# Performance work log

Hardware: AMD Instinct MI355X
Metric: run time of the kernel (lower is better)

## Reference

```python
import jax, jax.numpy as jnp
import numpy as np

B, S, V, E, H = 1024, 64, 32, 256, 512
META = 13


def setup_inputs() -> dict:
    key = jax.random.key(0)
    ks = jax.random.split(key, 12)
    return {
        "image_representation": jax.random.normal(ks[0], (B, META), jnp.float32),
        "messages": jax.random.randint(ks[1], (B, S), 0, V),
        "embedding": jax.random.normal(ks[2], (V, E), jnp.float32) * 0.1,
        "w_ih": jax.random.normal(ks[3], (4 * H, E), jnp.float32) * 0.02,
        "w_hh": jax.random.normal(ks[4], (4 * H, H), jnp.float32) * 0.02,
        "b_ih": jnp.zeros((4 * H,), jnp.float32),
        "b_hh": jnp.zeros((4 * H,), jnp.float32).at[H:2 * H].set(1.0),
        "proc_w": jax.random.normal(ks[5], (H, META), jnp.float32) * 0.1,
        "proc_b": jnp.zeros((H,), jnp.float32),
        "w1": jax.random.normal(ks[6], (H, 2 * H), jnp.float32) * 0.02,
        "b1": jnp.zeros((H,), jnp.float32),
        "w2": jax.random.normal(ks[7], (2, H), jnp.float32) * 0.02,
        "b2": jnp.zeros((2,), jnp.float32),
    }


def _lstm_run(emb_tbe, w_ih, w_hh, b_ih, b_hh):
    # emb_tbe: [S, B, E]; PyTorch LSTMCell gate order: i, f, g, o
    Bn = emb_tbe.shape[1]
    Hn = w_hh.shape[1]

    def step(carry, x_t):
        h, c = carry
        gates = x_t @ w_ih.T + b_ih + h @ w_hh.T + b_hh  # [B, 4H]
        i, f, g, o = jnp.split(gates, 4, axis=-1)
        c = jax.nn.sigmoid(f) * c + jax.nn.sigmoid(i) * jnp.tanh(g)
        h = jax.nn.sigmoid(o) * jnp.tanh(c)
        return (h, c), None

    init = (jnp.zeros((Bn, Hn), emb_tbe.dtype), jnp.zeros((Bn, Hn), emb_tbe.dtype))
    (h, _), _ = jax.lax.scan(step, init, emb_tbe)
    return h


def reference(image_representation, messages, embedding, w_ih, w_hh, b_ih, b_hh,
              proc_w, proc_b, w1, b1, w2, b2):
    emb = embedding[messages]                       # [B, S, E]
    h = _lstm_run(jnp.transpose(emb, (1, 0, 2)), w_ih, w_hh, b_ih, b_hh)  # [B, H]
    img = image_representation @ proc_w.T + proc_b  # [B, H]
    combined = jnp.concatenate([h, img], axis=1)    # [B, 2H]
    hidden = jax.nn.relu(combined @ w1.T + b1)
    prediction = hidden @ w2.T + b2                 # [B, 2]
    return prediction, emb
```

## Files before the change

### kernel.cpp

```cpp
#include <hip/hip_runtime.h>

typedef __attribute__((ext_vector_type(8))) short bf16x8;
typedef __attribute__((ext_vector_type(4))) float f32x4;
typedef unsigned long long u64;

__device__ __forceinline__ unsigned short f2bf(float x) {
    union { float f; unsigned u; } c; c.f = x;
    unsigned u = c.u + 0x7fffu + ((c.u >> 16) & 1u);
    return (unsigned short)(u >> 16);
}
__device__ __forceinline__ unsigned pack2(float a, float b) {
    return (unsigned)f2bf(a) | ((unsigned)f2bf(b) << 16);
}
__device__ __forceinline__ float sigm(float x) { return 1.f / (1.f + __expf(-x)); }
__device__ __forceinline__ float tanh_(float x) { return 1.f - 2.f / (__expf(2.f * x) + 1.f); }

#define ALOAD(p)     __hip_atomic_load((p), __ATOMIC_RELAXED, __HIP_MEMORY_SCOPE_AGENT)
#define ASTORE(p, v) __hip_atomic_store((p), (v), __ATOMIC_RELAXED, __HIP_MEMORY_SCOPE_AGENT)

__global__ __launch_bounds__(256) void prep_k(
    const float* __restrict__ emb, const float* __restrict__ w_ih,
    const float* __restrict__ b_ih, const float* __restrict__ b_hh,
    const float* __restrict__ w_hh, const float* __restrict__ w1,
    const float* __restrict__ imgr, const float* __restrict__ procw,
    const float* __restrict__ procb,
    float* __restrict__ table, unsigned short* __restrict__ Wp,
    unsigned short* __restrict__ w1p, unsigned short* __restrict__ imgb)
{
    int wg = blockIdx.x, tid = threadIdx.x;
    if (wg < 256) {
        int id = wg * 256 + tid;
        int v = id >> 11, c = id & 2047;
        int c7 = c & 127, tt = c >> 7;
        int srow = ((c7 >> 4) & 3) * 512 + tt * 32 + ((c7 >> 6) & 1) * 16 + (c7 & 15);
        const float4* e4 = (const float4*)(emb + v * 256);
        const float4* w4 = (const float4*)(w_ih + srow * 256);
        float a = 0.f;
        #pragma unroll 8
        for (int k = 0; k < 64; ++k) {
            float4 x = e4[k], y = w4[k];
            a += x.x * y.x + x.y * y.y + x.z * y.z + x.w * y.w;
        }
        table[id] = a + b_ih[srow] + b_hh[srow];
    } else if (wg < 768) {
        int id = (wg - 256) * 256 + tid;
        int c = id >> 6, j = id & 63;
        int c7 = c & 127, tt = c >> 7;
        int srow = ((c7 >> 4) & 3) * 512 + tt * 32 + ((c7 >> 6) & 1) * 16 + (c7 & 15);
        const float4* s4 = (const float4*)(w_hh + srow * 512 + j * 8);
        float4 x = s4[0], y = s4[1];
        uint4 r;
        r.x = pack2(x.x, x.y); r.y = pack2(x.z, x.w);
        r.z = pack2(y.x, y.y); r.w = pack2(y.z, y.w);
        *(uint4*)(Wp + c * 512 + j * 8) = r;
    } else if (wg < 1024) {
        int id = (wg - 768) * 256 + tid;
        const float4* s4 = (const float4*)(w1 + id * 8);
        float4 x = s4[0], y = s4[1];
        uint4 r;
        r.x = pack2(x.x, x.y); r.y = pack2(x.z, x.w);
        r.z = pack2(y.x, y.y); r.w = pack2(y.z, y.w);
        *(uint4*)(w1p + id * 8) = r;
    } else {
        int id = (wg - 1024) * 256 + tid;
        int b = id >> 9, h = id & 511;
        const float* ir = imgr + b * 13;
        const float* pw = procw + h * 13;
        float a = procb[h];
        #pragma unroll
        for (int k = 0; k < 13; ++k) a += ir[k] * pw[k];
        imgb[id] = f2bf(a);
    }
}

template<int FAST>
__device__ __forceinline__ void steps_loop(
    const uint4* BshF, const float* Tsh, const unsigned char* Msh,
    unsigned short* Hsh, u64* hb, unsigned* myflag, int g, int t)
{
    const int tid = threadIdx.x;
    const int lane = tid & 63, wid = tid >> 6;
    const int wr = wid >> 1, wc = wid & 1;
    const int l15 = lane & 15, l4 = lane >> 4;
    const int arow = g * 64 + wr * 16 + l15;
    const int bbase = wc * 4096;
    float creg[4] = {0.f, 0.f, 0.f, 0.f};

    for (int s = 0; s < 64; ++s) {
        f32x4 acc[4] = {};
        if (s > 0) {
            const unsigned tgt = (unsigned)s;
            for (;;) {
                unsigned v = ALOAD(&myflag[l15]);
                if (__all((int)(v >= tgt))) break;
                __builtin_amdgcn_s_sleep(1);
            }
            asm volatile("" ::: "memory");
            const u64* hp = hb + (size_t)((s - 1) & 7) * 131072;
            u64 a0[16], a1[16];
            #pragma unroll
            for (int kg = 0; kg < 16; ++kg) {
                int idx = arow * 128 + kg * 8 + l4 * 2;
                if (FAST) { a0[kg] = hp[idx];         a1[kg] = hp[idx + 1]; }
                else      { a0[kg] = ALOAD(&hp[idx]); a1[kg] = ALOAD(&hp[idx + 1]); }
            }
            #pragma unroll
            for (int kg = 0; kg < 16; ++kg) {
                union { u64 u[2]; bf16x8 v; } A;
                A.u[0] = a0[kg]; A.u[1] = a1[kg];
                #pragma unroll
                for (int cf = 0; cf < 4; ++cf) {
                    bf16x8 bfr = *(const bf16x8*)&BshF[bbase + (kg * 4 + cf) * 64 + lane];
                    acc[cf] = __builtin_amdgcn_mfma_f32_16x16x32_bf16(
                        A.v, bfr, acc[cf], 0, 0, 0);
                }
            }
        }
        #pragma unroll
        for (int reg = 0; reg < 4; ++reg) {
            int bl = wr * 16 + l4 * 4 + reg;
            int v = Msh[s * 64 + bl];
            const float* tr = Tsh + v * 128 + wc * 64 + l15;
            float gi = acc[0][reg] + tr[0];
            float gf = acc[1][reg] + tr[16];
            float gg = acc[2][reg] + tr[32];
            float go = acc[3][reg] + tr[48];
            float cn = sigm(gf) * creg[reg] + sigm(gi) * tanh_(gg);
            creg[reg] = cn;
            Hsh[bl * 40 + wc * 16 + l15] = f2bf(sigm(go) * tanh_(cn));
        }
        __syncthreads();
        {
            int row = tid >> 3, j = tid & 7;
            u64 val = *(const u64*)&Hsh[row * 40 + j * 4];
            u64* hw = hb + (size_t)(s & 7) * 131072;
            if (FAST) hw[(g * 64 + row) * 128 + t * 8 + j] = val;
            else      ASTORE(&hw[(g * 64 + row) * 128 + t * 8 + j], val);
        }
        __syncthreads();
        if (tid == 0) ASTORE(&myflag[t], (unsigned)(s + 1));
    }
}

__global__ __launch_bounds__(512, 2) void lstm_k(
    const float* __restrict__ table, const unsigned short* __restrict__ Wp,
    const int* __restrict__ msgs, u64* __restrict__ hb,
    unsigned* __restrict__ flags)
{
    extern __shared__ char smem[];
    uint4* BshF = (uint4*)smem;
    float* Tsh  = (float*)(smem + 131072);
    unsigned char* Msh = (unsigned char*)(smem + 147456);
    unsigned short* Hsh = (unsigned short*)(smem + 151552);

    const int tid = threadIdx.x;
    const int x = blockIdx.x;
    const int g = (x & 7) | (((x >> 7) & 1) << 3);
    const int t = (x >> 3) & 15;

    const uint4* wg4 = (const uint4*)Wp;
    #pragma unroll
    for (int it = 0; it < 16; ++it) {
        int p = it * 512 + tid;
        int col = p >> 6, ks = p & 63;
        uint4 v = wg4[(t * 128 + col) * 64 + ks];
        int dst = (((col >> 6) * 16 + (ks >> 2)) * 4 + ((col >> 4) & 3)) * 64
                  + (ks & 3) * 16 + (col & 15);
        BshF[dst] = v;
    }
    const uint4* tg = (const uint4*)table;
    uint4* T4 = (uint4*)Tsh;
    #pragma unroll
    for (int it = 0; it < 2; ++it) {
        int p = it * 512 + tid;
        T4[p] = tg[(p >> 5) * 512 + t * 32 + (p & 31)];
    }
    #pragma unroll
    for (int it = 0; it < 8; ++it) {
        int p = it * 512 + tid;
        int row = p >> 6, s_ = p & 63;
        Msh[s_ * 64 + row] = (unsigned char)msgs[(g * 64 + row) * 64 + s_];
    }
    __syncthreads();

    unsigned* xslots = flags + 256;
    unsigned* verd   = flags + 512;
    volatile unsigned* bc = (volatile unsigned*)Hsh;
    if (tid == 0) {
        unsigned xcd;
        asm volatile("s_getreg_b32 %0, hwreg(HW_REG_XCC_ID)" : "=s"(xcd));
        ASTORE(&xslots[g * 16 + t], xcd + 1u);
        if (t == 0) {
            unsigned ok = 1, first = 0;
            long spins = 0;
            for (int i = 0; i < 16 && ok; ++i) {
                unsigned v;
                for (;;) {
                    v = ALOAD(&xslots[g * 16 + i]);
                    if (v) break;
                    if (++spins > (1 << 20)) { ok = 0; break; }
                    __builtin_amdgcn_s_sleep(2);
                }
                if (!ok) break;
                if (i == 0) first = v;
                else if (v != first) ok = 0;
            }
            ASTORE(&verd[g], ok + 1u);
        }
        unsigned v;
        do {
            v = ALOAD(&verd[g]);
            if (!v) __builtin_amdgcn_s_sleep(2);
        } while (!v);
        bc[0] = v - 1;
    }
    __syncthreads();
    unsigned fastu = bc[0];
    __syncthreads();

    unsigned* myflag = flags + g * 16;
    if (fastu) steps_loop<1>(BshF, Tsh, Msh, Hsh, hb, myflag, g, t);
    else       steps_loop<0>(BshF, Tsh, Msh, Hsh, hb, myflag, g, t);
}

__global__ __launch_bounds__(256) void mlp2_k(
    const u64* __restrict__ hfin, const unsigned short* __restrict__ imgb,
    const unsigned short* __restrict__ w1p, const float* __restrict__ b1,
    float* __restrict__ hid)
{
    __shared__ uint4 ldsA[512];
    __shared__ uint4 ldsB[256];
    const int tid = threadIdx.x;
    const int lane = tid & 63, wid = tid >> 6;
    const int l15 = lane & 15, l4 = lane >> 4;
    const int mbase = blockIdx.y * 64;
    const int t = blockIdx.x;

    const uint4* h4 = (const uint4*)hfin;
    const uint4* ia = (const uint4*)imgb;
    const uint4* wb = (const uint4*)w1p;

    f32x4 acc[2] = {};
    uint4 ra[2], rb1;

    #pragma unroll
    for (int j = 0; j < 2; ++j) {
        int p = tid + j * 256, row = p >> 3, ss = (p & 7) ^ (row & 7);
        ra[j] = h4[(mbase + row) * 64 + ss];
    }
    {
        int col = tid >> 3, ss = (tid & 7) ^ (col & 7);
        rb1 = wb[(t * 32 + col) * 128 + ss];
    }
    #pragma unroll
    for (int j = 0; j < 2; ++j) ldsA[tid + j * 256] = ra[j];
    ldsB[tid] = rb1;
    __syncthreads();

    for (int kc = 0; kc < 16; ++kc) {
        if (kc < 15) {
            int kn = kc + 1;
            #pragma unroll
            for (int j = 0; j < 2; ++j) {
                int p = tid + j * 256, row = p >> 3, ss = (p & 7) ^ (row & 7);
                ra[j] = (kn < 8) ? h4[(mbase + row) * 64 + kn * 8 + ss]
                                 : ia[(mbase + row) * 64 + (kn - 8) * 8 + ss];
            }
            int col = tid >> 3, ss = (tid & 7) ^ (col & 7);
            rb1 = wb[(t * 32 + col) * 128 + kn * 8 + ss];
        }
        #pragma unroll
        for (int kg = 0; kg < 2; ++kg) {
            int row = wid * 16 + l15;
            bf16x8 af = *(const bf16x8*)&ldsA[row * 8 + ((kg * 4 + l4) ^ (row & 7))];
            #pragma unroll
            for (int cf = 0; cf < 2; ++cf) {
                int col = cf * 16 + l15;
                bf16x8 bf = *(const bf16x8*)&ldsB[col * 8 + ((kg * 4 + l4) ^ (col & 7))];
                acc[cf] = __builtin_amdgcn_mfma_f32_16x16x32_bf16(af, bf, acc[cf], 0, 0, 0);
            }
        }
        if (kc < 15) {
            __syncthreads();
            #pragma unroll
            for (int j = 0; j < 2; ++j) ldsA[tid + j * 256] = ra[j];
            ldsB[tid] = rb1;
            __syncthreads();
        }
    }

    #pragma unroll
    for (int reg = 0; reg < 4; ++reg) {
        int b = mbase + wid * 16 + l4 * 4 + reg;
        #pragma unroll
        for (int cf = 0; cf < 2; ++cf) {
            int n = t * 32 + cf * 16 + l15;
            hid[b * 512 + n] = fmaxf(acc[cf][reg] + b1[n], 0.f);
        }
    }
}

__global__ __launch_bounds__(256) void pred2_k(
    const float* __restrict__ hid, const float* __restrict__ w2,
    const float* __restrict__ b2, float* __restrict__ out)
{
    int wid = threadIdx.x >> 6, lane = threadIdx.x & 63;
    int b = blockIdx.x * 4 + wid;
    const float4* hr = (const float4*)(hid + b * 512);
    const float4* wA = (const float4*)(w2);
    const float4* wB = (const float4*)(w2 + 512);
    float a0 = 0.f, a1 = 0.f;
    #pragma unroll
    for (int j = 0; j < 2; ++j) {
        float4 h4 = hr[lane * 2 + j];
        float4 x0 = wA[lane * 2 + j], x1 = wB[lane * 2 + j];
        a0 += h4.x * x0.x + h4.y * x0.y + h4.z * x0.z + h4.w * x0.w;
        a1 += h4.x * x1.x + h4.y * x1.y + h4.z * x1.z + h4.w * x1.w;
    }
    #pragma unroll
    for (int off = 32; off > 0; off >>= 1) {
        a0 += __shfl_xor(a0, off);
        a1 += __shfl_xor(a1, off);
    }
    if (lane == 0) {
        out[b * 2]     = a0 + b2[0];
        out[b * 2 + 1] = a1 + b2[1];
    }
}

__global__ __launch_bounds__(256) void gather_k(
    const float* __restrict__ emb, const int* __restrict__ msgs,
    float* __restrict__ out)
{
    const float4* e4 = (const float4*)emb;
    float4* o4 = (float4*)out;
    int id = blockIdx.x * 256 + threadIdx.x;
    #pragma unroll
    for (int it = 0; it < 4; ++it) {
        int p = id + it * 1048576;
        int bs = p >> 6, e = p & 63;
        int v = msgs[bs];
        o4[p] = e4[v * 64 + e];
    }
}

extern "C" void kernel_launch(void* const* d_in, const int* in_sizes, int n_in,
                              void* d_out, int out_size, void* d_ws, size_t ws_size,
                              hipStream_t stream)
{
    const float* imgr  = (const float*)d_in[0];
    const int*   msgs  = (const int*)d_in[1];
    const float* emb   = (const float*)d_in[2];
    const float* w_ih  = (const float*)d_in[3];
    const float* w_hh  = (const float*)d_in[4];
    const float* b_ih  = (const float*)d_in[5];
    const float* b_hh  = (const float*)d_in[6];
    const float* procw = (const float*)d_in[7];
    const float* procb = (const float*)d_in[8];
    const float* w1    = (const float*)d_in[9];
    const float* b1    = (const float*)d_in[10];
    const float* w2    = (const float*)d_in[11];
    const float* b2    = (const float*)d_in[12];
    float* outp = (float*)d_out;

    const size_t OFF_WP   = 262144;
    const size_t OFF_H    = 2359296;
    const size_t OFF_IMGB = OFF_H + 8388608;
    const size_t OFF_W1P  = OFF_IMGB + 1048576;
    const size_t OFF_HID  = OFF_W1P + 1048576;
    const size_t OFF_FLG  = OFF_HID + 2097152;
    const size_t NEED     = OFF_FLG + 4096;
    char* ws = (ws_size >= NEED) ? (char*)d_ws : (char*)(outp + 2048);

    float*          table = (float*)(ws);
    unsigned short* Wp    = (unsigned short*)(ws + OFF_WP);
    u64*            hb    = (u64*)(ws + OFF_H);
    unsigned short* imgb  = (unsigned short*)(ws + OFF_IMGB);
    unsigned short* w1p   = (unsigned short*)(ws + OFF_W1P);
    float*          hid   = (float*)(ws + OFF_HID);
    unsigned*       flags = (unsigned*)(ws + OFF_FLG);

    hipMemsetAsync(flags, 0, 4096, stream);
    hipFuncSetAttribute((const void*)lstm_k,
                        hipFuncAttributeMaxDynamicSharedMemorySize, 156672);

    prep_k<<<3072, 256, 0, stream>>>(emb, w_ih, b_ih, b_hh, w_hh, w1, imgr,
                                     procw, procb, table, Wp, w1p, imgb);
    lstm_k<<<256, 512, 156672, stream>>>(table, Wp, msgs, hb, flags);
    mlp2_k<<<dim3(16, 16), 256, 0, stream>>>(hb + (size_t)7 * 131072, imgb,
                                             w1p, b1, hid);
    pred2_k<<<256, 256, 0, stream>>>(hid, w2, b2, outp);
    gather_k<<<4096, 256, 0, stream>>>(emb, msgs, outp + 2048);
}
```

Before: 459.7 us.

## Pad per-block flags to separate cache lines and prefetch ready h slices incrementally

Each producer block's step flag now sits on its own 128-byte line instead of being packed together, which avoids contention on a shared cache line. In the fast path, each block no longer waits for all 16 producers before loading h. It polls the flags and loads each producer's slice of the previous hidden state into registers as soon as that producer signals, so the global loads overlap with the wait. This adds 16 persistent uint4 registers per lane and a polling loop after every step, which may raise register pressure in the occupancy-2 kernel.

```diff
diff --git a/kernel.cpp b/kernel.cpp
--- a/kernel.cpp
+++ b/kernel.cpp
@@ -76,7 +76,7 @@
 template<int FAST>
 __device__ __forceinline__ void steps_loop(
     const uint4* BshF, const float* Tsh, const unsigned char* Msh,
-    unsigned short* Hsh, u64* hb, unsigned* myflag, int g, int t)
+    unsigned short* Hsh, u64* hb, unsigned* flags_g, int g, int t)
 {
     const int tid = threadIdx.x;
     const int lane = tid & 63, wid = tid >> 6;
@@ -85,36 +85,41 @@
     const int arow = g * 64 + wr * 16 + l15;
     const int bbase = wc * 4096;
     float creg[4] = {0.f, 0.f, 0.f, 0.f};
+    uint4 A0 = {}, A1 = {}, A2 = {}, A3 = {}, A4 = {}, A5 = {}, A6 = {}, A7 = {};
+    uint4 A8 = {}, A9 = {}, A10 = {}, A11 = {}, A12 = {}, A13 = {}, A14 = {}, A15 = {};
 
     for (int s = 0; s < 64; ++s) {
         f32x4 acc[4] = {};
         if (s > 0) {
-            const unsigned tgt = (unsigned)s;
-            for (;;) {
-                unsigned v = ALOAD(&myflag[l15]);
-                if (__all((int)(v >= tgt))) break;
-                __builtin_amdgcn_s_sleep(1);
+            if (!FAST) {
+                const unsigned tgt = (unsigned)s;
+                for (;;) {
+                    unsigned v = ALOAD(&flags_g[l15 * 32]);
+                    if (__all((int)(v >= tgt))) break;
+                    __builtin_amdgcn_s_sleep(1);
+                }
+                asm volatile("" ::: "memory");
+                const u64* hp8 = hb + (size_t)((s - 1) & 7) * 131072;
+                #define SLD(i) { u64 q0 = ALOAD(&hp8[arow * 128 + i * 8 + l4 * 2]); \
+                                 u64 q1 = ALOAD(&hp8[arow * 128 + i * 8 + l4 * 2 + 1]); \
+                                 A##i = make_uint4((unsigned)q0, (unsigned)(q0 >> 32), \
+                                                   (unsigned)q1, (unsigned)(q1 >> 32)); }
+                SLD(0) SLD(1) SLD(2) SLD(3) SLD(4) SLD(5) SLD(6) SLD(7)
+                SLD(8) SLD(9) SLD(10) SLD(11) SLD(12) SLD(13) SLD(14) SLD(15)
+                #undef SLD
             }
-            asm volatile("" ::: "memory");
-            const u64* hp = hb + (size_t)((s - 1) & 7) * 131072;
-            u64 a0[16], a1[16];
-            #pragma unroll
-            for (int kg = 0; kg < 16; ++kg) {
-                int idx = arow * 128 + kg * 8 + l4 * 2;
-                if (FAST) { a0[kg] = hp[idx];         a1[kg] = hp[idx + 1]; }
-                else      { a0[kg] = ALOAD(&hp[idx]); a1[kg] = ALOAD(&hp[idx + 1]); }
-            }
-            #pragma unroll
-            for (int kg = 0; kg < 16; ++kg) {
-                union { u64 u[2]; bf16x8 v; } A;
-                A.u[0] = a0[kg]; A.u[1] = a1[kg];
-                #pragma unroll
-                for (int cf = 0; cf < 4; ++cf) {
-                    bf16x8 bfr = *(const bf16x8*)&BshF[bbase + (kg * 4 + cf) * 64 + lane];
-                    acc[cf] = __builtin_amdgcn_mfma_f32_16x16x32_bf16(
-                        A.v, bfr, acc[cf], 0, 0, 0);
-                }
-            }
+            #define MFS(i) { bf16x8 af = *(const bf16x8*)&A##i; \
+                acc[0] = __builtin_amdgcn_mfma_f32_16x16x32_bf16(af, \
+                    *(const bf16x8*)&BshF[bbase + (i * 4 + 0) * 64 + lane], acc[0], 0, 0, 0); \
+                acc[1] = __builtin_amdgcn_mfma_f32_16x16x32_bf16(af, \
+                    *(const bf16x8*)&BshF[bbase + (i * 4 + 1) * 64 + lane], acc[1], 0, 0, 0); \
+                acc[2] = __builtin_amdgcn_mfma_f32_16x16x32_bf16(af, \
+                    *(const bf16x8*)&BshF[bbase + (i * 4 + 2) * 64 + lane], acc[2], 0, 0, 0); \
+                acc[3] = __builtin_amdgcn_mfma_f32_16x16x32_bf16(af, \
+                    *(const bf16x8*)&BshF[bbase + (i * 4 + 3) * 64 + lane], acc[3], 0, 0, 0); }
+            MFS(0) MFS(1) MFS(2) MFS(3) MFS(4) MFS(5) MFS(6) MFS(7)
+            MFS(8) MFS(9) MFS(10) MFS(11) MFS(12) MFS(13) MFS(14) MFS(15)
+            #undef MFS
         }
         #pragma unroll
         for (int reg = 0; reg < 4; ++reg) {
@@ -137,8 +142,32 @@
             if (FAST) hw[(g * 64 + row) * 128 + t * 8 + j] = val;
             else      ASTORE(&hw[(g * 64 + row) * 128 + t * 8 + j], val);
         }
+        unsigned vv0 = 0;
+        if (FAST && s < 63) vv0 = ALOAD(&flags_g[l15 * 32]);
         __syncthreads();
-        if (tid == 0) ASTORE(&myflag[t], (unsigned)(s + 1));
+        if (tid == 0) ASTORE(&flags_g[t * 32], (unsigned)(s + 1));
+        if (FAST && s < 63) {
+            const unsigned tgt = (unsigned)(s + 1);
+            const uint4* hn = (const uint4*)(hb + (size_t)(s & 7) * 131072);
+            unsigned done = (((unsigned)__ballot((int)(vv0 >= tgt))) & 0xFFFFu) | (1u << t);
+            asm volatile("" ::: "memory");
+            #define FLD(i) if ((done >> i) & 1) A##i = hn[arow * 64 + i * 4 + l4];
+            FLD(0) FLD(1) FLD(2) FLD(3) FLD(4) FLD(5) FLD(6) FLD(7)
+            FLD(8) FLD(9) FLD(10) FLD(11) FLD(12) FLD(13) FLD(14) FLD(15)
+            #undef FLD
+            while (done != 0xFFFFu) {
+                unsigned vv = ALOAD(&flags_g[l15 * 32]);
+                unsigned rdy = (((unsigned)__ballot((int)(vv >= tgt))) & 0xFFFFu) & ~done;
+                if (rdy) {
+                    asm volatile("" ::: "memory");
+                    #define FLD(i) if ((rdy >> i) & 1) A##i = hn[arow * 64 + i * 4 + l4];
+                    FLD(0) FLD(1) FLD(2) FLD(3) FLD(4) FLD(5) FLD(6) FLD(7)
+                    FLD(8) FLD(9) FLD(10) FLD(11) FLD(12) FLD(13) FLD(14) FLD(15)
+                    #undef FLD
+                    done |= rdy;
+                }
+            }
+        }
     }
 }
 
@@ -183,8 +212,8 @@
     }
     __syncthreads();
 
-    unsigned* xslots = flags + 256;
-    unsigned* verd   = flags + 512;
+    unsigned* xslots = flags + 8192;
+    unsigned* verd   = flags + 8448;
     volatile unsigned* bc = (volatile unsigned*)Hsh;
     if (tid == 0) {
         unsigned xcd;
@@ -218,9 +247,9 @@
     unsigned fastu = bc[0];
     __syncthreads();
 
-    unsigned* myflag = flags + g * 16;
-    if (fastu) steps_loop<1>(BshF, Tsh, Msh, Hsh, hb, myflag, g, t);
-    else       steps_loop<0>(BshF, Tsh, Msh, Hsh, hb, myflag, g, t);
+    unsigned* flags_g = flags + g * 512;
+    if (fastu) steps_loop<1>(BshF, Tsh, Msh, Hsh, hb, flags_g, g, t);
+    else       steps_loop<0>(BshF, Tsh, Msh, Hsh, hb, flags_g, g, t);
 }
 
 __global__ __launch_bounds__(256) void mlp2_k(
@@ -369,7 +398,7 @@
     const size_t OFF_W1P  = OFF_IMGB + 1048576;
     const size_t OFF_HID  = OFF_W1P + 1048576;
     const size_t OFF_FLG  = OFF_HID + 2097152;
-    const size_t NEED     = OFF_FLG + 4096;
+    const size_t NEED     = OFF_FLG + 36864;
     char* ws = (ws_size >= NEED) ? (char*)d_ws : (char*)(outp + 2048);
 
     float*          table = (float*)(ws);
@@ -380,7 +409,7 @@
     float*          hid   = (float*)(ws + OFF_HID);
     unsigned*       flags = (unsigned*)(ws + OFF_FLG);
 
-    hipMemsetAsync(flags, 0, 4096, stream);
+    hipMemsetAsync(flags, 0, 36864, stream);
     hipFuncSetAttribute((const void*)lstm_k,
                         hipFuncAttributeMaxDynamicSharedMemorySize, 156672);
 
```

Result: slower. 545.8 us (+18.7%).
